# Kernel optimization log

Hardware: AMD Instinct MI355X
Metric: run time of the kernel (lower is better)

Reference implementation:

```python
import jax, jax.numpy as jnp
import numpy as np

B, N, DIM = 2, 2048, 1024
HEADS, DIM_HEAD = 8, 64
INNER = HEADS * DIM_HEAD  # 512
EPS = 1e-5  # fp32 branch of the source LayerNorm


def setup_inputs() -> dict:
    key = jax.random.key(0)
    ks = jax.random.split(key, 5)
    x = jax.random.normal(ks[0], (B, N, DIM), dtype=jnp.float32)
    g = jnp.ones((DIM,), dtype=jnp.float32)  # LayerNorm gain init
    # Linear weights stored as (in, out) so y = x @ W. Source zero-inits
    # to_out; we use small random values so the baseline output is nonzero.
    wq = jax.random.normal(ks[1], (DIM, INNER), dtype=jnp.float32) * 0.02
    wkv = jax.random.normal(ks[2], (DIM, 2 * INNER), dtype=jnp.float32) * 0.02
    wo = jax.random.normal(ks[3], (INNER, DIM), dtype=jnp.float32) * 0.02
    return {"x": x, "g": g, "wq": wq, "wkv": wkv, "wo": wo}


def reference(x, g, wq, wkv, wo):
    # Custom LayerNorm from the source: statistics over dim=1 (sequence axis!)
    mean = jnp.mean(x, axis=1, keepdims=True)
    var = jnp.var(x, axis=1, keepdims=True)  # unbiased=False
    xn = (x - mean) * jax.lax.rsqrt(var + EPS) * g  # g broadcasts on last dim

    q = xn @ wq                      # [b, n, inner]
    kv = xn @ wkv                    # [b, n, 2*inner]
    k, v = jnp.split(kv, 2, axis=-1)

    def split_heads(t):  # b n (h d) -> b h n d
        b, n, _ = t.shape
        return t.reshape(b, n, HEADS, DIM_HEAD).transpose(0, 2, 1, 3)

    q, k, v = map(split_heads, (q, k, v))
    q = q * (DIM_HEAD ** -0.5)

    sim = jnp.einsum('bhid,bhjd->bhij', q, k)   # [b, h, n, n]
    attn = jax.nn.softmax(sim, axis=-1)
    out = jnp.einsum('bhij,bhjd->bhid', attn, v)  # [b, h, n, d]

    out = out.transpose(0, 2, 1, 3).reshape(B, N, INNER)  # b h n d -> b n (h d)
    return out @ wo  # [b, n, dim]
```

## Files before the change

kernel.cpp:

```cpp
#include <hip/hip_runtime.h>
#include <hip/hip_bf16.h>
#include <stdint.h>


#define B_ 2
#define N_ 2048
#define DIM_ 1024
#define DH_ 64
#define INNER_ 512
#define ROWS_ 4096
#define POSTRIDE 2097152

#define QSCALE 0.18033688011112042f

typedef __bf16 bf16x8 __attribute__((ext_vector_type(8)));
typedef float floatx4 __attribute__((ext_vector_type(4)));

#if __has_builtin(__builtin_amdgcn_exp2f)
#define EXP2(x) __builtin_amdgcn_exp2f(x)
#else
#define EXP2(x) exp2f(x)
#endif

__device__ __forceinline__ ushort f2bf(float f) {
    union { float f; uint32_t u; } v; v.f = f;
    uint32_t u = v.u;
    u += 0x7fffu + ((u >> 16) & 1u);
    return (ushort)(u >> 16);
}
__device__ __forceinline__ uint32_t pkbf(float a, float b) {
    return (uint32_t)f2bf(a) | ((uint32_t)f2bf(b) << 16);
}
__device__ __forceinline__ void gld_lds(const ushort* g, ushort* l) {
    __builtin_amdgcn_global_load_lds(
        (const __attribute__((address_space(1))) void*)g,
        (__attribute__((address_space(3))) void*)l, 16, 0, 0);
}
__device__ __forceinline__ size_t frag_off(int m, int k, int nkc) {
    return ((size_t)((m >> 4) * nkc + (k >> 5)) * 64 +
            (size_t)((m & 15) | (((k >> 3) & 3) << 4))) * 8 + (k & 7);
}

__global__ __launch_bounds__(256) void setup_fused(
    const float* __restrict__ x, float* __restrict__ ps, float* __restrict__ pq,
    const float* __restrict__ wq, const float* __restrict__ wkv,
    const float* __restrict__ wo, ushort* __restrict__ wqkv_f,
    ushort* __restrict__ wo_f) {
    __shared__ float tile[32][33];
    int bid = blockIdx.x;
    if (bid < 256) {
        int gd = (bid & 7) * 256 + threadIdx.x;
        int ch = bid >> 3;
        int b = gd >> 10;
        const float* p = x + (size_t)(b * N_ + ch * 64) * DIM_ + (gd & 1023);
        float s = 0.f, q = 0.f;
#pragma unroll 4
        for (int n = 0; n < 64; ++n) { float v = p[(size_t)n * DIM_]; s += v; q += v * v; }
        ps[ch * 2048 + gd] = s;
        pq[ch * 2048 + gd] = q;
        return;
    }
    int t = bid - 256;
    const float* src; ushort* dst; int C, K, k0, ncol0, nglob0; float scale;
    if (t < 512) {
        int kt = t >> 4, nt = t & 15;
        src = wq; dst = wqkv_f; C = 512; K = 1024; scale = QSCALE;
        k0 = kt * 32; ncol0 = nt * 32; nglob0 = ncol0;
    } else if (t < 1536) {
        int u = t - 512; int kt = u >> 5, nt = u & 31;
        src = wkv; dst = wqkv_f; C = 1024; K = 1024; scale = 1.f;
        k0 = kt * 32; ncol0 = nt * 32; nglob0 = 512 + ncol0;
    } else {
        int u = t - 1536; int kt = u >> 5, nt = u & 31;
        src = wo; dst = wo_f; C = 1024; K = 512; scale = 1.f;
        k0 = kt * 32; ncol0 = nt * 32; nglob0 = ncol0;
    }
    int ti = threadIdx.x >> 5, tj = threadIdx.x & 31;
#pragma unroll
    for (int p = 0; p < 4; ++p)
        tile[ti + 8 * p][tj] = src[(size_t)(k0 + ti + 8 * p) * C + ncol0 + tj] * scale;
    __syncthreads();
    if (threadIdx.x < 128) {
        int nl = threadIdx.x & 31, kc8 = threadIdx.x >> 5;
        union { ushort us[8]; uint4 v; } u;
#pragma unroll
        for (int ii = 0; ii < 8; ++ii) u.us[ii] = f2bf(tile[kc8 * 8 + ii][nl]);
        *(uint4*)&dst[frag_off(nglob0 + nl, k0 + kc8 * 8, K >> 5)] = u.v;
    }
}

__global__ __launch_bounds__(256) void finalize_norm(
    const float* __restrict__ ps, const float* __restrict__ pq,
    const float* __restrict__ x, const float* __restrict__ g,
    ushort* __restrict__ xnf) {
    __shared__ float s4[4][64], q4[4][64], aa[64], bb[64];
    int t = threadIdx.x;
    int b = blockIdx.x >> 8, slab = (blockIdx.x >> 4) & 15, nch = blockIdx.x & 15;
    int c0 = slab * 64;
    {
        int c = t & 63, grp = t >> 6;
        float s = 0.f, q = 0.f;
#pragma unroll
        for (int ch = 0; ch < 8; ++ch) {
            int o = (grp * 8 + ch) * 2048 + b * 1024 + c0 + c;
            s += ps[o]; q += pq[o];
        }
        s4[grp][c] = s; q4[grp][c] = q;
    }
    __syncthreads();
    if (t < 64) {
        float s = s4[0][t] + s4[1][t] + s4[2][t] + s4[3][t];
        float q = q4[0][t] + q4[1][t] + q4[2][t] + q4[3][t];
        float mean = s * (1.f / N_);
        float var = q * (1.f / N_) - mean * mean;
        float rstd = rsqrtf(var + 1e-5f);
        float a = rstd * g[c0 + t];
        aa[t] = a; bb[t] = -mean * a;
    }
    __syncthreads();
    int c4 = (t & 15) * 4, ro = t >> 4;
#pragma unroll
    for (int it = 0; it < 8; ++it) {
        int r = nch * 128 + it * 16 + ro;
        int m = b * 2048 + r;
        float4 xv = *(const float4*)&x[(size_t)m * DIM_ + c0 + c4];
        float v0 = xv.x * aa[c4 + 0] + bb[c4 + 0];
        float v1 = xv.y * aa[c4 + 1] + bb[c4 + 1];
        float v2 = xv.z * aa[c4 + 2] + bb[c4 + 2];
        float v3 = xv.w * aa[c4 + 3] + bb[c4 + 3];
        uint2 u; u.x = pkbf(v0, v1); u.y = pkbf(v2, v3);
        *(uint2*)&xnf[frag_off(m, c0 + c4, 32)] = u;
    }
}

template <int NKC>
__device__ __forceinline__ void gemm_core(
    const ushort* __restrict__ pA, const ushort* __restrict__ pB,
    floatx4 (&acc)[4][4]) {
    constexpr int TS = NKC * 512;
    bf16x8 a0[4], b0[4], a1[4], b1[4];
#pragma unroll
    for (int i = 0; i < 4; ++i) {
        a0[i] = *(const bf16x8*)(pA + (size_t)i * TS);
        b0[i] = *(const bf16x8*)(pB + (size_t)i * TS);
    }
    for (int kc = 0; kc < NKC; kc += 2) {
#pragma unroll
        for (int i = 0; i < 4; ++i) {
            a1[i] = *(const bf16x8*)(pA + (size_t)i * TS + (size_t)(kc + 1) * 512);
            b1[i] = *(const bf16x8*)(pB + (size_t)i * TS + (size_t)(kc + 1) * 512);
        }
#pragma unroll
        for (int mi = 0; mi < 4; ++mi)
#pragma unroll
            for (int ni = 0; ni < 4; ++ni)
                acc[mi][ni] = __builtin_amdgcn_mfma_f32_16x16x32_bf16(
                    a0[mi], b0[ni], acc[mi][ni], 0, 0, 0);
        if (kc + 2 < NKC) {
#pragma unroll
            for (int i = 0; i < 4; ++i) {
                a0[i] = *(const bf16x8*)(pA + (size_t)i * TS + (size_t)(kc + 2) * 512);
                b0[i] = *(const bf16x8*)(pB + (size_t)i * TS + (size_t)(kc + 2) * 512);
            }
        }
#pragma unroll
        for (int mi = 0; mi < 4; ++mi)
#pragma unroll
            for (int ni = 0; ni < 4; ++ni)
                acc[mi][ni] = __builtin_amdgcn_mfma_f32_16x16x32_bf16(
                    a1[mi], b1[ni], acc[mi][ni], 0, 0, 0);
    }
}

__global__ __launch_bounds__(128) void gemm_qkv(
    const ushort* __restrict__ xnf, const ushort* __restrict__ wf,
    ushort* __restrict__ qk, ushort* __restrict__ vT) {
    int tx = threadIdx.x, w = tx >> 6, l = tx & 63;
    int lr = l & 15, lq = l >> 4;
    int bx = blockIdx.x, by = blockIdx.y;
    const ushort* pA = xnf + (size_t)(bx * 4) * 32 * 512 + l * 8;
    const ushort* pB = wf + (size_t)(by * 8 + w * 4) * 32 * 512 + l * 8;
    floatx4 acc[4][4] = {};
    gemm_core<32>(pA, pB, acc);
    int col0 = by * 128 + w * 64;
    if (by < 8) {
#pragma unroll
        for (int mi = 0; mi < 4; ++mi)
#pragma unroll
            for (int ni = 0; ni < 4; ++ni) {
                int col = col0 + 16 * ni + lr;
#pragma unroll
                for (int reg = 0; reg < 4; ++reg) {
                    int row = bx * 64 + 16 * mi + 4 * lq + reg;
                    qk[(size_t)row * 1024 + col] = f2bf(acc[mi][ni][reg]);
                }
            }
    } else {
#pragma unroll
        for (int mi = 0; mi < 4; ++mi) {
            int row0 = bx * 64 + 16 * mi + 4 * lq;
            int bb2 = row0 >> 11, nn = row0 & 2047;
#pragma unroll
            for (int ni = 0; ni < 4; ++ni) {
                int cv = col0 - 1024 + 16 * ni + lr;
                int h = cv >> 6, d = cv & 63;
                uint2 u;
                u.x = pkbf(acc[mi][ni][0], acc[mi][ni][1]);
                u.y = pkbf(acc[mi][ni][2], acc[mi][ni][3]);
                *(uint2*)&vT[((size_t)((bb2 * 8 + h) * 64 + d)) * 2048 + nn] = u;
            }
        }
    }
}

__global__ __launch_bounds__(128) void gemm_out(
    const ushort* __restrict__ af, const ushort* __restrict__ wf,
    float* __restrict__ out) {
    int tx = threadIdx.x, w = tx >> 6, l = tx & 63;
    int lr = l & 15, lq = l >> 4;
    int bx = blockIdx.x, by = blockIdx.y;
    const ushort* pA = af + (size_t)(bx * 4) * 16 * 512 + l * 8;
    const ushort* pB = wf + (size_t)(by * 8 + w * 4) * 16 * 512 + l * 8;
    floatx4 acc[4][4] = {};
    gemm_core<16>(pA, pB, acc);
    int col0 = by * 128 + w * 64;
#pragma unroll
    for (int mi = 0; mi < 4; ++mi)
#pragma unroll
        for (int ni = 0; ni < 4; ++ni) {
            int col = col0 + 16 * ni + lr;
#pragma unroll
            for (int reg = 0; reg < 4; ++reg) {
                int row = bx * 64 + 16 * mi + 4 * lq + reg;
                out[(size_t)row * 1024 + col] = acc[mi][ni][reg];
            }
        }
}

__global__ __launch_bounds__(256, 4) void flash_attn(
    const ushort* __restrict__ qk, const ushort* __restrict__ vT,
    float* __restrict__ po, float* __restrict__ pl, int nkt) {
    __shared__ __align__(16) ushort sK[64 * 64];
    __shared__ __align__(16) ushort sV[64 * 64];
    __shared__ __align__(16) ushort sPQ[4 * 32 * 72];

    const int tx = threadIdx.x;
    const int w = tx >> 6, l = tx & 63;
    const int lr = l & 15, lq = l >> 4;
    const int qt = blockIdx.x, bh = blockIdx.y, sp = blockIdx.z;
    const int b = bh >> 3, h = bh & 7;
    const size_t rowbase = (size_t)b * N_;
    const int qbase = qt * 128;
    const int kbase = sp * nkt * 64;

    const int rl = l >> 3;
    const int swz8 = ((l & 7) ^ rl) * 8;
    const int fr0 = (lq ^ (lr & 7)) * 8;
    const int fr1 = ((4 + lq) ^ (lr & 7)) * 8;

#pragma unroll
    for (int i = 0; i < 4; ++i) {
        int r0 = 32 * w + 8 * i;
        gld_lds(qk + (rowbase + qbase + r0 + rl) * 1024 + h * DH_ + swz8,
                &sPQ[r0 * 64]);
    }
    __syncthreads();
    bf16x8 bq[2][2];
#pragma unroll
    for (int qq = 0; qq < 2; ++qq) {
        int r = (32 * w + 16 * qq + lr) * 64;
        bq[qq][0] = *(const bf16x8*)&sPQ[r + fr0];
        bq[qq][1] = *(const bf16x8*)&sPQ[r + fr1];
    }

    floatx4 o[2][4] = {};
    float lsum[2] = {0.f, 0.f};

    for (int kt = 0; kt < nkt; ++kt) {
        __syncthreads();
#pragma unroll
        for (int i = 0; i < 2; ++i) {
            int r0 = 16 * w + 8 * i;
            gld_lds(qk + (rowbase + kbase + kt * 64 + r0 + rl) * 1024 + 512 + h * DH_ + swz8,
                    &sK[r0 * 64]);
            gld_lds(vT + ((size_t)bh * DH_ + r0 + rl) * N_ + kbase + kt * 64 + swz8,
                    &sV[r0 * 64]);
        }
        __syncthreads();

        floatx4 c[4][2] = {};
#pragma unroll
        for (int s = 0; s < 2; ++s) {
            const int fo = s ? fr1 : fr0;
            bf16x8 ak[4];
#pragma unroll
            for (int kk = 0; kk < 4; ++kk)
                ak[kk] = *(const bf16x8*)&sK[(16 * kk + lr) * 64 + fo];
#pragma unroll
            for (int kk = 0; kk < 4; ++kk)
#pragma unroll
                for (int qq = 0; qq < 2; ++qq)
                    c[kk][qq] = __builtin_amdgcn_mfma_f32_16x16x32_bf16(
                        ak[kk], bq[qq][s], c[kk][qq], 0, 0, 0);
        }

#pragma unroll
        for (int kk = 0; kk < 4; ++kk)
#pragma unroll
            for (int qq = 0; qq < 2; ++qq) {
                float e0 = EXP2(c[kk][qq][0]);
                float e1 = EXP2(c[kk][qq][1]);
                float e2 = EXP2(c[kk][qq][2]);
                float e3 = EXP2(c[kk][qq][3]);
                lsum[qq] += (e0 + e1) + (e2 + e3);
                uint2 u; u.x = pkbf(e0, e1); u.y = pkbf(e2, e3);
                *(uint2*)&sPQ[(32 * w + 16 * qq + lr) * 72 + 16 * kk + 4 * lq] = u;
            }

#pragma unroll
        for (int s = 0; s < 2; ++s) {
            const int fo = s ? fr1 : fr0;
            bf16x8 ap[2], bv[4];
#pragma unroll
            for (int mi = 0; mi < 2; ++mi)
                ap[mi] = *(const bf16x8*)&sPQ[(32 * w + 16 * mi + lr) * 72 + 32 * s + 8 * lq];
#pragma unroll
            for (int dt = 0; dt < 4; ++dt)
                bv[dt] = *(const bf16x8*)&sV[(16 * dt + lr) * 64 + fo];
#pragma unroll
            for (int mi = 0; mi < 2; ++mi)
#pragma unroll
                for (int dt = 0; dt < 4; ++dt)
                    o[mi][dt] = __builtin_amdgcn_mfma_f32_16x16x32_bf16(
                        ap[mi], bv[dt], o[mi][dt], 0, 0, 0);
        }
    }

#pragma unroll
    for (int qq = 0; qq < 2; ++qq) {
        lsum[qq] += __shfl_xor(lsum[qq], 16);
        lsum[qq] += __shfl_xor(lsum[qq], 32);
    }
    float* pob = po + (size_t)sp * POSTRIDE;
    if (lq == 0) {
#pragma unroll
        for (int qq = 0; qq < 2; ++qq)
            pl[((size_t)sp * 16 + bh) * N_ + qbase + 32 * w + 16 * qq + lr] = lsum[qq];
    }
    const size_t obase = (size_t)bh * N_;
#pragma unroll
    for (int mi = 0; mi < 2; ++mi)
#pragma unroll
        for (int dt = 0; dt < 4; ++dt)
#pragma unroll
            for (int reg = 0; reg < 4; ++reg) {
                int row = qbase + 32 * w + 16 * mi + 4 * lq + reg;
                pob[(obase + row) * DH_ + 16 * dt + lr] = o[mi][dt][reg];
            }
}

__global__ __launch_bounds__(256) void merge_attn(
    const float* __restrict__ po, const float* __restrict__ pl,
    ushort* __restrict__ attnf, int nsplit) {
    int idx = blockIdx.x * 256 + threadIdx.x;
    int d4 = (idx & 15) * 4;
    int h = (idx >> 4) & 7;
    int rowg = idx >> 7;
    int b = rowg >> 11, r = rowg & 2047;
    size_t pbase = ((size_t)b * 8 + h) * N_ + r;
    float4 acc = *(const float4*)&po[pbase * DH_ + d4];
    float lv = pl[pbase];
    for (int s = 1; s < nsplit; ++s) {
        float4 a1 = *(const float4*)&po[(size_t)s * POSTRIDE + pbase * DH_ + d4];
        acc.x += a1.x; acc.y += a1.y; acc.z += a1.z; acc.w += a1.w;
        lv += pl[((size_t)s * 16) * N_ + pbase];
    }
    float inv = 1.f / lv;
    uint2 u;
    u.x = pkbf(acc.x * inv, acc.y * inv);
    u.y = pkbf(acc.z * inv, acc.w * inv);
    *(uint2*)&attnf[frag_off(rowg, h * DH_ + d4, 16)] = u;
}

extern "C" void kernel_launch(void* const* d_in, const int* in_sizes, int n_in,
                              void* d_out, int out_size, void* d_ws, size_t ws_size,
                              hipStream_t stream) {
    const float* x   = (const float*)d_in[0];
    const float* g   = (const float*)d_in[1];
    const float* wq  = (const float*)d_in[2];
    const float* wkv = (const float*)d_in[3];
    const float* wo  = (const float*)d_in[4];
    float* out = (float*)d_out;

    char* ws = (char*)d_ws;
    float*  psum   = (float*)(ws + 0);
    float*  psqr   = (float*)(ws + 262144);
    ushort* xnf    = (ushort*)(ws + 524288);
    ushort* wqkv_f = (ushort*)(ws + 8912896);
    ushort* wo_f   = (ushort*)(ws + 12058624);
    ushort* qkb    = (ushort*)(ws + 13107200);
    ushort* vTb    = (ushort*)(ws + 21495808);
    ushort* attnf  = (ushort*)(ws + 25690112);
    float*  plb    = (float*)(ws + 29884416);
    float*  pob    = (float*)(ws + 30408704);

    const int nsplit = (ws_size >= (size_t)66 * 1024 * 1024) ? 4
                     : (ws_size >= (size_t)48 * 1024 * 1024) ? 2 : 1;

    setup_fused<<<2304, 256, 0, stream>>>(x, psum, psqr, wq, wkv, wo, wqkv_f, wo_f);
    finalize_norm<<<512, 256, 0, stream>>>(psum, psqr, x, g, xnf);
    gemm_qkv<<<dim3(64, 12), 128, 0, stream>>>(xnf, wqkv_f, qkb, vTb);
    flash_attn<<<dim3(16, 16, nsplit), 256, 0, stream>>>(qkb, vTb, pob, plb, 32 / nsplit);
    merge_attn<<<2048, 256, 0, stream>>>(pob, plb, attnf, nsplit);
    gemm_out<<<dim3(64, 8), 128, 0, stream>>>(attnf, wo_f, out);
}
```

Before: 158.8 us.

## Write Q/K/V in MFMA fragment layout and load K/V directly to registers

The QKV GEMM epilogue now writes Q, K and V into per-head buffers already arranged in MFMA fragment order. The attention kernel can then load K and V fragments straight from global memory into registers with a two-deep software double buffer, instead of staging them through LDS behind barriers. Only the P tile still uses LDS, and it is per-wave, so the block-level syncs are removed. The cost is that each wave re-reads K/V from global memory or L2 without sharing across waves, and register pressure rises, which is why occupancy is lowered to 2 blocks per CU.

```diff
diff --git a/kernel.cpp b/kernel.cpp
--- a/kernel.cpp
+++ b/kernel.cpp
@@ -10,6 +10,7 @@
 #define INNER_ 512
 #define ROWS_ 4096
 #define POSTRIDE 2097152
+#define BHSTRIDE 131072
 
 #define QSCALE 0.18033688011112042f
 
@@ -30,11 +31,6 @@
 }
 __device__ __forceinline__ uint32_t pkbf(float a, float b) {
     return (uint32_t)f2bf(a) | ((uint32_t)f2bf(b) << 16);
-}
-__device__ __forceinline__ void gld_lds(const ushort* g, ushort* l) {
-    __builtin_amdgcn_global_load_lds(
-        (const __attribute__((address_space(1))) void*)g,
-        (__attribute__((address_space(3))) void*)l, 16, 0, 0);
 }
 __device__ __forceinline__ size_t frag_off(int m, int k, int nkc) {
     return ((size_t)((m >> 4) * nkc + (k >> 5)) * 64 +
@@ -174,7 +170,7 @@
 
 __global__ __launch_bounds__(128) void gemm_qkv(
     const ushort* __restrict__ xnf, const ushort* __restrict__ wf,
-    ushort* __restrict__ qk, ushort* __restrict__ vT) {
+    ushort* __restrict__ qf, ushort* __restrict__ kf, ushort* __restrict__ vf) {
     int tx = threadIdx.x, w = tx >> 6, l = tx & 63;
     int lr = l & 15, lq = l >> 4;
     int bx = blockIdx.x, by = blockIdx.y;
@@ -183,31 +179,38 @@
     floatx4 acc[4][4] = {};
     gemm_core<32>(pA, pB, acc);
     int col0 = by * 128 + w * 64;
+    int bb2 = (bx * 64) >> 11;
     if (by < 8) {
-#pragma unroll
-        for (int mi = 0; mi < 4; ++mi)
-#pragma unroll
-            for (int ni = 0; ni < 4; ++ni) {
-                int col = col0 + 16 * ni + lr;
-#pragma unroll
-                for (int reg = 0; reg < 4; ++reg) {
-                    int row = bx * 64 + 16 * mi + 4 * lq + reg;
-                    qk[(size_t)row * 1024 + col] = f2bf(acc[mi][ni][reg]);
-                }
-            }
+        ushort* qkbase = (by < 4) ? qf : kf;
+#pragma unroll
+        for (int ni = 0; ni < 4; ++ni) {
+            int col = col0 + 16 * ni + lr;
+            int hh = (col >> 6) & 7, d = col & 63;
+            ushort* base = qkbase + (size_t)(bb2 * 8 + hh) * BHSTRIDE
+                           + (d >> 5) * 512 + ((d >> 3) & 3) * 128 + (d & 7)
+                           + (4 * lq) * 8;
+#pragma unroll
+            for (int mi = 0; mi < 4; ++mi) {
+                size_t o2 = (size_t)((bx * 4 + mi) & 127) * 1024;
+#pragma unroll
+                for (int reg = 0; reg < 4; ++reg)
+                    base[o2 + reg * 8] = f2bf(acc[mi][ni][reg]);
+            }
+        }
     } else {
 #pragma unroll
-        for (int mi = 0; mi < 4; ++mi) {
-            int row0 = bx * 64 + 16 * mi + 4 * lq;
-            int bb2 = row0 >> 11, nn = row0 & 2047;
-#pragma unroll
-            for (int ni = 0; ni < 4; ++ni) {
-                int cv = col0 - 1024 + 16 * ni + lr;
-                int h = cv >> 6, d = cv & 63;
+        for (int ni = 0; ni < 4; ++ni) {
+            int cv = col0 - 1024 + 16 * ni + lr;
+            int hh = cv >> 6, d = cv & 63;
+            ushort* base = vf + (size_t)(bb2 * 8 + hh) * BHSTRIDE
+                           + (d >> 4) * 32768 + (d & 15) * 8;
+#pragma unroll
+            for (int mi = 0; mi < 4; ++mi) {
+                int nn = (bx * 64 + 16 * mi + 4 * lq) & 2047;
                 uint2 u;
                 u.x = pkbf(acc[mi][ni][0], acc[mi][ni][1]);
                 u.y = pkbf(acc[mi][ni][2], acc[mi][ni][3]);
-                *(uint2*)&vT[((size_t)((bb2 * 8 + h) * 64 + d)) * 2048 + nn] = u;
+                *(uint2*)&base[(nn >> 5) * 512 + ((nn >> 3) & 3) * 128 + (nn & 7)] = u;
             }
         }
     }
@@ -237,73 +240,59 @@
         }
 }
 
-__global__ __launch_bounds__(256, 4) void flash_attn(
-    const ushort* __restrict__ qk, const ushort* __restrict__ vT,
-    float* __restrict__ po, float* __restrict__ pl, int nkt) {
-    __shared__ __align__(16) ushort sK[64 * 64];
-    __shared__ __align__(16) ushort sV[64 * 64];
-    __shared__ __align__(16) ushort sPQ[4 * 32 * 72];
+__global__ __launch_bounds__(256, 2) void flash_attn(
+    const ushort* __restrict__ qf, const ushort* __restrict__ kf,
+    const ushort* __restrict__ vf, float* __restrict__ po,
+    float* __restrict__ pl, int nkt) {
+    __shared__ __align__(16) ushort sP[4][32 * 72];
 
     const int tx = threadIdx.x;
     const int w = tx >> 6, l = tx & 63;
     const int lr = l & 15, lq = l >> 4;
     const int qt = blockIdx.x, bh = blockIdx.y, sp = blockIdx.z;
-    const int b = bh >> 3, h = bh & 7;
-    const size_t rowbase = (size_t)b * N_;
     const int qbase = qt * 128;
     const int kbase = sp * nkt * 64;
 
-    const int rl = l >> 3;
-    const int swz8 = ((l & 7) ^ rl) * 8;
-    const int fr0 = (lq ^ (lr & 7)) * 8;
-    const int fr1 = ((4 + lq) ^ (lr & 7)) * 8;
-
-#pragma unroll
-    for (int i = 0; i < 4; ++i) {
-        int r0 = 32 * w + 8 * i;
-        gld_lds(qk + (rowbase + qbase + r0 + rl) * 1024 + h * DH_ + swz8,
-                &sPQ[r0 * 64]);
-    }
-    __syncthreads();
+    const ushort* qfb = qf + (size_t)bh * BHSTRIDE + (size_t)(qbase + 32 * w) * 64 + l * 8;
+    const ushort* kfb = kf + (size_t)bh * BHSTRIDE + (size_t)kbase * 64 + l * 8;
+    const ushort* vfb = vf + (size_t)bh * BHSTRIDE + (size_t)kbase * 16 + l * 8;
+    ushort* sPw = &sP[w][0];
+
     bf16x8 bq[2][2];
 #pragma unroll
-    for (int qq = 0; qq < 2; ++qq) {
-        int r = (32 * w + 16 * qq + lr) * 64;
-        bq[qq][0] = *(const bf16x8*)&sPQ[r + fr0];
-        bq[qq][1] = *(const bf16x8*)&sPQ[r + fr1];
-    }
+    for (int qq = 0; qq < 2; ++qq)
+#pragma unroll
+        for (int s = 0; s < 2; ++s)
+            bq[qq][s] = *(const bf16x8*)(qfb + qq * 1024 + s * 512);
 
     floatx4 o[2][4] = {};
     float lsum[2] = {0.f, 0.f};
 
-    for (int kt = 0; kt < nkt; ++kt) {
-        __syncthreads();
-#pragma unroll
-        for (int i = 0; i < 2; ++i) {
-            int r0 = 16 * w + 8 * i;
-            gld_lds(qk + (rowbase + kbase + kt * 64 + r0 + rl) * 1024 + 512 + h * DH_ + swz8,
-                    &sK[r0 * 64]);
-            gld_lds(vT + ((size_t)bh * DH_ + r0 + rl) * N_ + kbase + kt * 64 + swz8,
-                    &sV[r0 * 64]);
-        }
-        __syncthreads();
-
+    bf16x8 ak[2][8], bv[2][8];
+    auto load_kv = [&](int kt, int buf) {
+        const ushort* kp = kfb + (size_t)kt * 4096;
+        const ushort* vp = vfb + (size_t)kt * 1024;
+#pragma unroll
+        for (int kk = 0; kk < 4; ++kk) {
+            ak[buf][kk * 2 + 0] = *(const bf16x8*)(kp + kk * 1024);
+            ak[buf][kk * 2 + 1] = *(const bf16x8*)(kp + kk * 1024 + 512);
+        }
+#pragma unroll
+        for (int dt = 0; dt < 4; ++dt) {
+            bv[buf][dt * 2 + 0] = *(const bf16x8*)(vp + dt * 32768);
+            bv[buf][dt * 2 + 1] = *(const bf16x8*)(vp + dt * 32768 + 512);
+        }
+    };
+    auto compute = [&](int buf) {
         floatx4 c[4][2] = {};
 #pragma unroll
-        for (int s = 0; s < 2; ++s) {
-            const int fo = s ? fr1 : fr0;
-            bf16x8 ak[4];
-#pragma unroll
-            for (int kk = 0; kk < 4; ++kk)
-                ak[kk] = *(const bf16x8*)&sK[(16 * kk + lr) * 64 + fo];
+        for (int s = 0; s < 2; ++s)
 #pragma unroll
             for (int kk = 0; kk < 4; ++kk)
 #pragma unroll
                 for (int qq = 0; qq < 2; ++qq)
                     c[kk][qq] = __builtin_amdgcn_mfma_f32_16x16x32_bf16(
-                        ak[kk], bq[qq][s], c[kk][qq], 0, 0, 0);
-        }
-
+                        ak[buf][kk * 2 + s], bq[qq][s], c[kk][qq], 0, 0, 0);
 #pragma unroll
         for (int kk = 0; kk < 4; ++kk)
 #pragma unroll
@@ -314,27 +303,32 @@
                 float e3 = EXP2(c[kk][qq][3]);
                 lsum[qq] += (e0 + e1) + (e2 + e3);
                 uint2 u; u.x = pkbf(e0, e1); u.y = pkbf(e2, e3);
-                *(uint2*)&sPQ[(32 * w + 16 * qq + lr) * 72 + 16 * kk + 4 * lq] = u;
-            }
-
+                *(uint2*)&sPw[(16 * qq + lr) * 72 + 16 * kk + 4 * lq] = u;
+            }
 #pragma unroll
         for (int s = 0; s < 2; ++s) {
-            const int fo = s ? fr1 : fr0;
-            bf16x8 ap[2], bv[4];
+            bf16x8 ap[2];
 #pragma unroll
             for (int mi = 0; mi < 2; ++mi)
-                ap[mi] = *(const bf16x8*)&sPQ[(32 * w + 16 * mi + lr) * 72 + 32 * s + 8 * lq];
-#pragma unroll
-            for (int dt = 0; dt < 4; ++dt)
-                bv[dt] = *(const bf16x8*)&sV[(16 * dt + lr) * 64 + fo];
+                ap[mi] = *(const bf16x8*)&sPw[(16 * mi + lr) * 72 + 32 * s + 8 * lq];
 #pragma unroll
             for (int mi = 0; mi < 2; ++mi)
 #pragma unroll
                 for (int dt = 0; dt < 4; ++dt)
                     o[mi][dt] = __builtin_amdgcn_mfma_f32_16x16x32_bf16(
-                        ap[mi], bv[dt], o[mi][dt], 0, 0, 0);
-        }
-    }
+                        ap[mi], bv[buf][dt * 2 + s], o[mi][dt], 0, 0, 0);
+        }
+    };
+
+    load_kv(0, 0);
+    int kt = 0;
+    for (; kt + 2 <= nkt; kt += 2) {
+        load_kv(kt + 1, 1);
+        compute(0);
+        if (kt + 2 < nkt) load_kv(kt + 2, 0);
+        compute(1);
+    }
+    if (kt < nkt) compute(0);
 
 #pragma unroll
     for (int qq = 0; qq < 2; ++qq) {
@@ -398,8 +392,9 @@
     ushort* xnf    = (ushort*)(ws + 524288);
     ushort* wqkv_f = (ushort*)(ws + 8912896);
     ushort* wo_f   = (ushort*)(ws + 12058624);
-    ushort* qkb    = (ushort*)(ws + 13107200);
-    ushort* vTb    = (ushort*)(ws + 21495808);
+    ushort* qfb    = (ushort*)(ws + 13107200);
+    ushort* kfb    = (ushort*)(ws + 17301504);
+    ushort* vfb    = (ushort*)(ws + 21495808);
     ushort* attnf  = (ushort*)(ws + 25690112);
     float*  plb    = (float*)(ws + 29884416);
     float*  pob    = (float*)(ws + 30408704);
@@ -409,8 +404,8 @@
 
     setup_fused<<<2304, 256, 0, stream>>>(x, psum, psqr, wq, wkv, wo, wqkv_f, wo_f);
     finalize_norm<<<512, 256, 0, stream>>>(psum, psqr, x, g, xnf);
-    gemm_qkv<<<dim3(64, 12), 128, 0, stream>>>(xnf, wqkv_f, qkb, vTb);
-    flash_attn<<<dim3(16, 16, nsplit), 256, 0, stream>>>(qkb, vTb, pob, plb, 32 / nsplit);
+    gemm_qkv<<<dim3(64, 12), 128, 0, stream>>>(xnf, wqkv_f, qfb, kfb, vfb);
+    flash_attn<<<dim3(16, 16, nsplit), 256, 0, stream>>>(qfb, kfb, vfb, pob, plb, 32 / nsplit);
     merge_attn<<<2048, 256, 0, stream>>>(pob, plb, attnf, nsplit);
     gemm_out<<<dim3(64, 8), 128, 0, stream>>>(attnf, wo_f, out);
 }
```

New measurement: 162.4 us. 1.02x slower.
